# Optimization experiments

Measured on AMD Instinct MI355X. Metric: run time of the kernel, lower is better.

The kernel has to match this reference:

```python
import jax, jax.numpy as jnp
import numpy as np

N_P = 2048   # personality nodes
N_W = 89     # word nodes (fixed by user_word_adj[:, :89])
N_ALL = N_P + N_W
B = 16384    # users
E2 = 768     # sentence embedding size
UW = 313     # 89 word cols + 224 extra cols -> 32 + 224 = 256 for share1


def setup_inputs() -> dict:
    key = jax.random.key(0)
    ks = jax.random.split(key, 20)
    rn = lambda k, s, sc=0.1: (jax.random.normal(k, s, jnp.float32) * sc)
    pern_adj = jax.random.randint(ks[2], (N_P, N_P), 0, 2, jnp.int32)
    pern_adj = pern_adj.at[jnp.arange(N_P), jnp.arange(N_P)].set(1)
    word_pern_adj = jax.random.randint(ks[3], (N_ALL, N_ALL), 0, 2, jnp.int32)
    word_pern_adj = word_pern_adj.at[jnp.arange(N_ALL), jnp.arange(N_ALL)].set(1)
    return dict(
        pern_feature=rn(ks[0], (N_P, 256), 1.0),
        word_feature=rn(ks[1], (N_W, 256), 1.0),
        pern_adj=pern_adj,
        word_pern_adj=word_pern_adj,
        user_word_adj=jax.random.uniform(ks[4], (B, UW), jnp.float32),
        sentence_embed=rn(ks[5], (B, E2), 1.0),
        w1=rn(ks[6], (8, 256, 32)), a_src1=rn(ks[7], (8, 32)), a_dst1=rn(ks[8], (8, 32)), bias1=jnp.zeros((32,), jnp.float32),
        w2=rn(ks[9], (8, 256, 32)), a_src2=rn(ks[10], (8, 32)), a_dst2=rn(ks[11], (8, 32)), bias2=jnp.zeros((32,), jnp.float32),
        W_s1=rn(ks[12], (256, 128)), b_s1=jnp.zeros((128,), jnp.float32),
        W_s2=rn(ks[13], (E2, 128)), b_s2=jnp.zeros((128,), jnp.float32),
        W_f1=rn(ks[14], (128, 64)), b_f1=jnp.zeros((64,), jnp.float32),
        W_fa=rn(ks[15], (256, 128)), b_fa=jnp.zeros((128,), jnp.float32),
        W_fb=rn(ks[16], (128, 5)), b_fb=jnp.zeros((5,), jnp.float32),
    )


def gat(h, adj, w, a_src, a_dst, bias):
    # h: (n, f_in); w: (H, f_in, f_out); a_src/a_dst: (H, f_out); adj: (n, n) 0/1
    hp = jnp.einsum('nf,hfo->hno', h, w)                      # (H, n, f_out)
    e_src = jnp.einsum('hno,ho->hn', hp, a_src)               # (H, n)
    e_dst = jnp.einsum('hno,ho->hn', hp, a_dst)               # (H, n)
    e = jax.nn.leaky_relu(e_src[:, :, None] + e_dst[:, None, :], 0.2)  # (H, n, n)
    e = jnp.where(adj[None, :, :] > 0, e, jnp.float32(-1e9))
    attn = jax.nn.softmax(e, axis=-1)
    out = jnp.einsum('hnm,hmo->hno', attn, hp) + bias         # (H, n, f_out)
    return out, attn


def reference(pern_feature, word_feature, pern_adj, word_pern_adj,
              user_word_adj, sentence_embed,
              w1, a_src1, a_dst1, bias1, w2, a_src2, a_dst2, bias2,
              W_s1, b_s1, W_s2, b_s2, W_f1, b_f1, W_fa, b_fa, W_fb, b_fb):
    n_p = pern_feature.shape[0]
    # GAT 1 on personality graph
    h1, attn_pp = gat(pern_feature, pern_adj, w1, a_src1, a_dst1, bias1)
    h1 = jax.nn.elu(jnp.transpose(h1, (1, 0, 2)).reshape(n_p, -1))   # (n_p, 256)
    # dropout is identity at eval time
    h1_wp = jnp.concatenate([word_feature, h1], axis=0)               # (n_w+n_p, 256)
    # GAT 2 on word-personality graph, mean over heads
    h2, attn_wp = gat(h1_wp, word_pern_adj, w2, a_src2, a_dst2, bias2)
    h2 = h2.mean(axis=0)                                              # (n_w+n_p, 32)
    h2_word = h2[:word_feature.shape[0], :]                           # (89, 32)
    # user aggregation over word adjacency + row normalization
    x = user_word_adj[:, :N_W] @ h2_word                              # (B, 32)
    x_c = jnp.concatenate([x, user_word_adj[:, N_W:]], axis=1)        # (B, 256)
    x = x_c / x_c.sum(axis=1, keepdims=True)
    # dual heads
    output1 = x @ W_s1 + b_s1
    output2 = sentence_embed @ W_s2 + b_s2
    output1_new = output1 @ W_f1 + b_f1
    output2_new = output2 @ W_f1 + b_f1
    x_temp = jnp.concatenate([output1, output2], axis=1)
    x_temp = jax.nn.relu(x_temp @ W_fa + b_fa) @ W_fb + b_fb
    return (output1_new, output2_new, x_temp, attn_pp, attn_wp, x)
```

## Files before the change

### kernel.cpp

```cpp
#include <hip/hip_runtime.h>
#include <cstdint>
#include <cstddef>

#define N_P 2048
#define N_W 89
#define N_ALLC 2137
#define BQ 16384
#define E2C 768

typedef __attribute__((ext_vector_type(8))) short short8;
typedef __attribute__((ext_vector_type(4))) float float4v;

__device__ __forceinline__ float waveMax(float v){
#pragma unroll
  for (int o = 32; o > 0; o >>= 1) v = fmaxf(v, __shfl_down(v, o, 64));
  return v;
}
__device__ __forceinline__ float waveSum(float v){
#pragma unroll
  for (int o = 32; o > 0; o >>= 1) v += __shfl_down(v, o, 64);
  return v;
}
__device__ __forceinline__ unsigned short f2bf(float f){
  union { float f; unsigned int u; } v; v.f = f;
  unsigned int u = v.u;
  unsigned int r = (u + 0x7FFFu + ((u >> 16) & 1u)) >> 16;
  return (unsigned short)r;
}
__device__ __forceinline__ short8 cvt8(const float* p){
  float4 f0 = *(const float4*)p;
  float4 f1 = *(const float4*)(p + 4);
  short8 a;
  a[0] = (short)f2bf(f0.x); a[1] = (short)f2bf(f0.y);
  a[2] = (short)f2bf(f0.z); a[3] = (short)f2bf(f0.w);
  a[4] = (short)f2bf(f1.x); a[5] = (short)f2bf(f1.y);
  a[6] = (short)f2bf(f1.z); a[7] = (short)f2bf(f1.w);
  return a;
}

__device__ __forceinline__ void wpk_one(const float* __restrict__ W,
                                        unsigned short* __restrict__ out,
                                        int K, int N, int idx){
  if (idx >= K * N) return;
  int k = idx / N, n = idx - k * N;
  out[((size_t)((k >> 5) * 4 + ((k >> 3) & 3)) * N + n) * 8 + (k & 7)] = f2bf(W[idx]);
}

__global__ __launch_bounds__(256) void repack_all(
    const float* __restrict__ Ws1, unsigned short* __restrict__ ws1pk,
    const float* __restrict__ Ws2, unsigned short* __restrict__ ws2pk,
    const float* __restrict__ Wf1, unsigned short* __restrict__ wf1pk,
    const float* __restrict__ Wfa, unsigned short* __restrict__ wfapk,
    const float* __restrict__ wf, float* __restrict__ h1wp)
{
  int b = blockIdx.x, t = threadIdx.x;
  if (b < 128) {
    wpk_one(Ws1, ws1pk, 256, 128, b * 256 + t);
  } else if (b < 512) {
    wpk_one(Ws2, ws2pk, 768, 128, (b - 128) * 256 + t);
  } else if (b < 544) {
    wpk_one(Wf1, wf1pk, 128, 64, (b - 512) * 256 + t);
  } else if (b < 672) {
    wpk_one(Wfa, wfapk, 256, 128, (b - 544) * 256 + t);
  } else {
    int idx = (b - 672) * 256 + t;
    if (idx < N_W * 256) h1wp[idx] = wf[idx];
  }
}

__device__ __forceinline__ void gemm32_body(
    const float* __restrict__ A, int lda, int M,
    const float* __restrict__ w8,
    float* __restrict__ C, int ldc,
    int rt, int ct)
{
  __shared__ __align__(16) float As[16][36];
  __shared__ __align__(16) float Bs[16][68];
  int t = threadIdx.x;
  int m0 = rt * 32, n0 = ct * 64;
  int bk = t >> 4, bn = (t & 15) * 4;
  int tm = t >> 4, tn = t & 15;
  float acc[2][4] = {};
  for (int k0 = 0; k0 < 256; k0 += 16) {
    if (t < 128) {
      int ar = t >> 2, ak = (t & 3) * 4;
      float4 av = {0.f, 0.f, 0.f, 0.f};
      int arow = m0 + ar;
      if (arow < M) av = *(const float4*)(A + (size_t)arow * lda + k0 + ak);
      As[ak][ar] = av.x; As[ak + 1][ar] = av.y; As[ak + 2][ar] = av.z; As[ak + 3][ar] = av.w;
    }
    int n = n0 + bn;
    float4 bv = *(const float4*)(w8 + ((n >> 5) << 13) + ((k0 + bk) << 5) + (n & 31));
    *(float4*)&Bs[bk][bn] = bv;
    __syncthreads();
#pragma unroll
    for (int kk = 0; kk < 16; ++kk) {
      float a0 = As[kk][tm * 2], a1 = As[kk][tm * 2 + 1];
      float4 b4 = *(const float4*)&Bs[kk][tn * 4];
      acc[0][0] += a0 * b4.x; acc[0][1] += a0 * b4.y;
      acc[0][2] += a0 * b4.z; acc[0][3] += a0 * b4.w;
      acc[1][0] += a1 * b4.x; acc[1][1] += a1 * b4.y;
      acc[1][2] += a1 * b4.z; acc[1][3] += a1 * b4.w;
    }
    __syncthreads();
  }
#pragma unroll
  for (int i = 0; i < 2; ++i) {
    int row = m0 + tm * 2 + i;
    if (row < M) {
      float4 v;
      v.x = acc[i][0]; v.y = acc[i][1]; v.z = acc[i][2]; v.w = acc[i][3];
      *(float4*)(C + (size_t)row * ldc + n0 + tn * 4) = v;
    }
  }
}

__global__ __launch_bounds__(256) void hp1_o2(
    const float* __restrict__ pf, const float* __restrict__ w1,
    float* __restrict__ hp1,
    const float* __restrict__ sent, const unsigned short* __restrict__ ws2pk,
    const float* __restrict__ bs2, unsigned short* __restrict__ o12bf)
{
  int b = blockIdx.x, t = threadIdx.x;
  if (b < 256) {
    gemm32_body(pf, 256, N_P, w1, hp1, 256, b >> 2, b & 3);
    return;
  }
  int rb = b - 256;
  int w = t >> 6, lane = t & 63;
  int col = lane & 15, quad = lane >> 4;
  int rowA = rb * 64 + w * 16 + col;
  const float* A = sent + (size_t)rowA * E2C;
  float4v acc[8];
#pragma unroll
  for (int i = 0; i < 8; ++i) acc[i] = (float4v){0.f, 0.f, 0.f, 0.f};
#pragma unroll 4
  for (int k0 = 0; k0 < E2C; k0 += 32) {
    short8 a = cvt8(A + k0 + quad * 8);
    const unsigned short* wb = ws2pk + ((size_t)((k0 >> 5) * 4 + quad) * 128 + col) * 8;
#pragma unroll
    for (int nt = 0; nt < 8; ++nt)
      acc[nt] = __builtin_amdgcn_mfma_f32_16x16x32_bf16(a, *(const short8*)(wb + nt * 128), acc[nt], 0, 0, 0);
  }
  int rbase = rb * 64 + w * 16 + quad * 4;
#pragma unroll
  for (int nt = 0; nt < 8; ++nt) {
    int c = nt * 16 + col;
    float bv = bs2[c];
#pragma unroll
    for (int r = 0; r < 4; ++r)
      o12bf[(size_t)(rbase + r) * 256 + 128 + c] = f2bf(acc[nt][r] + bv);
  }
}

__global__ __launch_bounds__(256) void gemm_hp2(
    const float* __restrict__ h1wp, const float* __restrict__ w2,
    float* __restrict__ hp2)
{
  int b = blockIdx.x;
  gemm32_body(h1wp, 256, N_ALLC, w2, hp2, 256, b >> 2, b & 3);
}

__global__ __launch_bounds__(256) void esrc_edst(
    const float* __restrict__ hp,
    const float* __restrict__ a_src,
    const float* __restrict__ a_dst,
    float* __restrict__ es, float* __restrict__ ed,
    unsigned short* __restrict__ hppk,
    float* __restrict__ h2w, const float* __restrict__ b2,
    int N, int do_pack)
{
  __shared__ float sa[256], sd[256];
  int t = threadIdx.x;
  sa[t] = a_src[t]; sd[t] = a_dst[t];
  __syncthreads();
  int idx = blockIdx.x * 256 + t;
  if (h2w != nullptr && idx < N_W * 32) h2w[idx] = b2[idx & 31];
  if (idx >= N * 8) return;
  int n = idx >> 3, h = idx & 7;
  const float* hpp = hp + (size_t)n * 256 + h * 32;
  const float* ap = sa + h * 32;
  const float* dp = sd + h * 32;
  float s = 0.f, d = 0.f;
  float hv[32];
#pragma unroll
  for (int o = 0; o < 32; ++o) { hv[o] = hpp[o]; s += hv[o] * ap[o]; d += hv[o] * dp[o]; }
  es[h * N + n] = s; ed[h * N + n] = d;
  if (do_pack) {
    unsigned short* dst = hppk + (size_t)h * (N_P * 32)
                        + (size_t)((n >> 5) * 4 + ((n >> 3) & 3)) * 256 + (n & 7);
#pragma unroll
    for (int o = 0; o < 32; ++o) dst[o * 8] = f2bf(hv[o]);
  }
}

__global__ __launch_bounds__(256) void attn_softmax(
    const float* __restrict__ es, const float* __restrict__ ed,
    const int* __restrict__ adj,
    float* __restrict__ attn,
    int N)
{
  int h = blockIdx.x, n = blockIdx.y;
  int t = threadIdx.x, lane = t & 63, wid = t >> 6;
  __shared__ float red[4];
  float esv = es[h * N + n];
  const float* edh = ed + (size_t)h * N;
  const int* arow = adj + (size_t)n * N;
  float v[9];
  float lmax = -3e38f;
#pragma unroll
  for (int i = 0; i < 9; ++i) {
    int m = i * 256 + t;
    float x = -3e38f;
    if (m < N) {
      float e = esv + edh[m];
      e = (e >= 0.f) ? e : 0.2f * e;
      x = (arow[m] > 0) ? e : -1e9f;
    }
    v[i] = x; lmax = fmaxf(lmax, x);
  }
  lmax = waveMax(lmax);
  if (lane == 0) red[wid] = lmax;
  __syncthreads();
  float gmax = fmaxf(fmaxf(red[0], red[1]), fmaxf(red[2], red[3]));
  __syncthreads();
  float lsum = 0.f;
#pragma unroll
  for (int i = 0; i < 9; ++i) {
    int m = i * 256 + t;
    if (m < N) { float p = __expf(v[i] - gmax); v[i] = p; lsum += p; }
  }
  lsum = waveSum(lsum);
  if (lane == 0) red[wid] = lsum;
  __syncthreads();
  float inv = 1.f / (red[0] + red[1] + red[2] + red[3]);
  float* out = attn + ((size_t)h * N + n) * N;
#pragma unroll
  for (int i = 0; i < 9; ++i) {
    int m = i * 256 + t;
    if (m < N) out[m] = v[i] * inv;
  }
}

__global__ __launch_bounds__(256) void pv1_mfma(
    const float* __restrict__ attn,
    const unsigned short* __restrict__ hppk,
    const float* __restrict__ bias,
    float* __restrict__ h1wp)
{
  __shared__ float red[2][16][33];
  int t = threadIdx.x, w = t >> 6, lane = t & 63;
  int col = lane & 15, quad = lane >> 4;
  int kh = w >> 1, rh = (w & 1) * 16;
  int h = blockIdx.y;
  int row0 = blockIdx.x * 32;
  int rowA = row0 + rh + col;
  const float* arow = attn + ((size_t)h * N_P + rowA) * N_P + kh * 1024;
  const unsigned short* wb0 = hppk + (size_t)h * (N_P * 32) + (size_t)kh * 32768;
  float4v acc0 = {0.f, 0.f, 0.f, 0.f}, acc1 = {0.f, 0.f, 0.f, 0.f};
#pragma unroll 4
  for (int kk = 0; kk < 1024; kk += 32) {
    short8 a = cvt8(arow + kk + quad * 8);
    const unsigned short* wb = wb0 + ((size_t)((kk >> 5) * 4 + quad) * 32 + col) * 8;
    short8 b0 = *(const short8*)(wb);
    short8 b1 = *(const short8*)(wb + 128);
    acc0 = __builtin_amdgcn_mfma_f32_16x16x32_bf16(a, b0, acc0, 0, 0, 0);
    acc1 = __builtin_amdgcn_mfma_f32_16x16x32_bf16(a, b1, acc1, 0, 0, 0);
  }
  if (kh == 1) {
#pragma unroll
    for (int r = 0; r < 4; ++r) {
      red[w & 1][quad * 4 + r][col] = acc0[r];
      red[w & 1][quad * 4 + r][16 + col] = acc1[r];
    }
  }
  __syncthreads();
  if (kh == 0) {
    int rbase = row0 + rh + quad * 4;
#pragma unroll
    for (int r = 0; r < 4; ++r) {
      float v0 = acc0[r] + red[w & 1][quad * 4 + r][col] + bias[col];
      float v1 = acc1[r] + red[w & 1][quad * 4 + r][16 + col] + bias[16 + col];
      v0 = (v0 > 0.f) ? v0 : expm1f(v0);
      v1 = (v1 > 0.f) ? v1 : expm1f(v1);
      float* dst = h1wp + (size_t)(N_W + rbase + r) * 256 + h * 32;
      dst[col] = v0; dst[16 + col] = v1;
    }
  }
}

__global__ __launch_bounds__(256) void pv2(
    const float* __restrict__ attn,
    const float* __restrict__ hp,
    float* __restrict__ h2w)
{
  int n = blockIdx.x, h = blockIdx.y;
  int t = threadIdx.x, g = t >> 5, o = t & 31;
  const float* arow = attn + ((size_t)h * N_ALLC + n) * N_ALLC;
  float acc = 0.f;
  for (int m = g; m < N_ALLC; m += 8) acc += arow[m] * hp[(size_t)m * 256 + h * 32 + o];
  __shared__ float pv[8][33];
  pv[g][o] = acc;
  __syncthreads();
  if (t < 32) {
    float s = 0.f;
#pragma unroll
    for (int gg = 0; gg < 8; ++gg) s += pv[gg][t];
    atomicAdd(&h2w[n * 32 + t], s * 0.125f);
  }
}

__global__ __launch_bounds__(256) void xnorm_kernel(
    const float* __restrict__ uwa,
    const float* __restrict__ h2w,
    float* __restrict__ xout)
{
  __shared__ float urow[4][320];
  __shared__ float sh2w[N_W * 32];
  __shared__ float px[4][2][32];
  __shared__ float xh[4][33];
  __shared__ float inv[4];
  int t = threadIdx.x;
  int b0 = blockIdx.x * 4;
  for (int i = t; i < N_W * 32; i += 256) sh2w[i] = h2w[i];
  for (int idx = t; idx < 4 * 313; idx += 256) {
    int r = idx / 313, j = idx - r * 313;
    urow[r][j] = uwa[(size_t)(b0 + r) * 313 + j];
  }
  __syncthreads();
  {
    int r = t >> 6, q = (t >> 5) & 1, o = t & 31;
    float s = 0.f;
    int i0 = q * 45, i1 = q ? N_W : 45;
    for (int i = i0; i < i1; ++i) s += urow[r][i] * sh2w[i * 32 + o];
    px[r][q][o] = s;
  }
  __syncthreads();
  if (t < 128) {
    int r = t >> 5, o = t & 31;
    xh[r][o] = px[r][0][o] + px[r][1][o];
  }
  __syncthreads();
  int lane = t & 63, w = t >> 6;
  float ls = 0.f;
  for (int c = lane; c < 256; c += 64) {
    float v = (c < 32) ? xh[w][c] : urow[w][89 + c - 32];
    ls += v;
  }
  ls = waveSum(ls);
  if (lane == 0) inv[w] = 1.f / ls;
  __syncthreads();
  for (int idx = t; idx < 1024; idx += 256) {
    int r = idx >> 8, c = idx & 255;
    float v = (c < 32) ? xh[r][c] : urow[r][89 + c - 32];
    xout[(size_t)(b0 + r) * 256 + c] = v * inv[r];
  }
}

__global__ __launch_bounds__(256) void tail2(
    const float* __restrict__ x,
    const unsigned short* __restrict__ o12bf,
    const unsigned short* __restrict__ ws1pk,
    const unsigned short* __restrict__ wf1pk,
    const unsigned short* __restrict__ wfapk,
    const float* __restrict__ bs1,
    const float* __restrict__ bf1,
    const float* __restrict__ bfa,
    const float* __restrict__ Wfb,
    const float* __restrict__ bfb,
    float* __restrict__ o1n, float* __restrict__ o2n, float* __restrict__ xt)
{
  __shared__ unsigned short o12s[64][264];
  __shared__ float sWfb[640];
  int t = threadIdx.x, w = t >> 6, lane = t & 63;
  int col = lane & 15, quad = lane >> 4;
  int row0 = blockIdx.x * 64;
  for (int i = t; i < 640; i += 256) sWfb[i] = Wfb[i];
#pragma unroll
  for (int i = 0; i < 4; ++i) {
    int cid = t + i * 256;
    int r = cid >> 4, c8 = cid & 15;
    *(short8*)&o12s[r][128 + c8 * 8] =
        *(const short8*)(o12bf + (size_t)(row0 + r) * 256 + 128 + c8 * 8);
  }
  {
    int rowA = row0 + w * 16 + col;
    const float* A = x + (size_t)rowA * 256;
    float4v acc[8];
#pragma unroll
    for (int i = 0; i < 8; ++i) acc[i] = (float4v){0.f, 0.f, 0.f, 0.f};
#pragma unroll
    for (int k0 = 0; k0 < 256; k0 += 32) {
      short8 a = cvt8(A + k0 + quad * 8);
      const unsigned short* wb = ws1pk + ((size_t)((k0 >> 5) * 4 + quad) * 128 + col) * 8;
#pragma unroll
      for (int nt = 0; nt < 8; ++nt)
        acc[nt] = __builtin_amdgcn_mfma_f32_16x16x32_bf16(a, *(const short8*)(wb + nt * 128), acc[nt], 0, 0, 0);
    }
    int rb = w * 16 + quad * 4;
#pragma unroll
    for (int nt = 0; nt < 8; ++nt) {
      int c = nt * 16 + col;
      float bv = bs1[c];
#pragma unroll
      for (int r = 0; r < 4; ++r)
        o12s[rb + r][c] = f2bf(acc[nt][r] + bv);
    }
  }
  __syncthreads();
  int lr = w * 16 + col;
  float4v aT[8], a1[4], a2[4];
#pragma unroll
  for (int i = 0; i < 8; ++i) aT[i] = (float4v){0.f, 0.f, 0.f, 0.f};
#pragma unroll
  for (int i = 0; i < 4; ++i) { a1[i] = (float4v){0.f, 0.f, 0.f, 0.f}; a2[i] = (float4v){0.f, 0.f, 0.f, 0.f}; }
#pragma unroll
  for (int k0 = 0; k0 < 128; k0 += 32) {
    short8 a = *(const short8*)&o12s[lr][k0 + quad * 8];
    const unsigned short* wbT = wfapk + ((size_t)((k0 >> 5) * 4 + quad) * 128 + col) * 8;
    const unsigned short* wb1 = wf1pk + ((size_t)((k0 >> 5) * 4 + quad) * 64 + col) * 8;
#pragma unroll
    for (int nt = 0; nt < 8; ++nt)
      aT[nt] = __builtin_amdgcn_mfma_f32_16x16x32_bf16(a, *(const short8*)(wbT + nt * 128), aT[nt], 0, 0, 0);
#pragma unroll
    for (int nt = 0; nt < 4; ++nt)
      a1[nt] = __builtin_amdgcn_mfma_f32_16x16x32_bf16(a, *(const short8*)(wb1 + nt * 128), a1[nt], 0, 0, 0);
  }
#pragma unroll
  for (int k0 = 128; k0 < 256; k0 += 32) {
    short8 a = *(const short8*)&o12s[lr][k0 + quad * 8];
    const unsigned short* wbT = wfapk + ((size_t)((k0 >> 5) * 4 + quad) * 128 + col) * 8;
    const unsigned short* wb1 = wf1pk + ((size_t)(((k0 - 128) >> 5) * 4 + quad) * 64 + col) * 8;
#pragma unroll
    for (int nt = 0; nt < 8; ++nt)
      aT[nt] = __builtin_amdgcn_mfma_f32_16x16x32_bf16(a, *(const short8*)(wbT + nt * 128), aT[nt], 0, 0, 0);
#pragma unroll
    for (int nt = 0; nt < 4; ++nt)
      a2[nt] = __builtin_amdgcn_mfma_f32_16x16x32_bf16(a, *(const short8*)(wb1 + nt * 128), a2[nt], 0, 0, 0);
  }
  int rbase = row0 + w * 16 + quad * 4;
#pragma unroll
  for (int nt = 0; nt < 4; ++nt) {
    int c = nt * 16 + col;
    float b1v = bf1[c];
#pragma unroll
    for (int r = 0; r < 4; ++r) {
      o1n[(size_t)(rbase + r) * 64 + c] = a1[nt][r] + b1v;
      o2n[(size_t)(rbase + r) * 64 + c] = a2[nt][r] + b1v;
    }
  }
  float xp[4][5] = {};
#pragma unroll
  for (int nt = 0; nt < 8; ++nt) {
    int c = nt * 16 + col;
    float bav = bfa[c];
#pragma unroll
    for (int r = 0; r < 4; ++r) {
      float tv = fmaxf(aT[nt][r] + bav, 0.f);
#pragma unroll
      for (int q = 0; q < 5; ++q) xp[r][q] += tv * sWfb[c * 5 + q];
    }
  }
#pragma unroll
  for (int m = 1; m <= 8; m <<= 1) {
#pragma unroll
    for (int r = 0; r < 4; ++r)
#pragma unroll
      for (int q = 0; q < 5; ++q) xp[r][q] += __shfl_xor(xp[r][q], m, 64);
  }
  if (col == 0) {
#pragma unroll
    for (int r = 0; r < 4; ++r)
#pragma unroll
      for (int q = 0; q < 5; ++q) xt[(size_t)(rbase + r) * 5 + q] = xp[r][q] + bfb[q];
  }
}

extern "C" void kernel_launch(void* const* d_in, const int* in_sizes, int n_in,
                              void* d_out, int out_size, void* d_ws, size_t ws_size,
                              hipStream_t stream)
{
  const float* pf   = (const float*)d_in[0];
  const float* wf   = (const float*)d_in[1];
  const int*   adj1 = (const int*)d_in[2];
  const int*   adj2 = (const int*)d_in[3];
  const float* uwa  = (const float*)d_in[4];
  const float* sent = (const float*)d_in[5];
  const float* w1   = (const float*)d_in[6];
  const float* as1  = (const float*)d_in[7];
  const float* ad1  = (const float*)d_in[8];
  const float* b1   = (const float*)d_in[9];
  const float* w2   = (const float*)d_in[10];
  const float* as2  = (const float*)d_in[11];
  const float* ad2  = (const float*)d_in[12];
  const float* b2   = (const float*)d_in[13];
  const float* Ws1  = (const float*)d_in[14];
  const float* bs1  = (const float*)d_in[15];
  const float* Ws2  = (const float*)d_in[16];
  const float* bs2  = (const float*)d_in[17];
  const float* Wf1  = (const float*)d_in[18];
  const float* bf1  = (const float*)d_in[19];
  const float* Wfa  = (const float*)d_in[20];
  const float* bfa  = (const float*)d_in[21];
  const float* Wfb  = (const float*)d_in[22];
  const float* bfb  = (const float*)d_in[23];

  float* ws = (float*)d_ws;
  float* hp1  = ws;
  float* hp2  = hp1 + (size_t)N_P * 256;
  float* es1v = hp2 + (size_t)N_ALLC * 256;
  float* ed1v = es1v + 8 * N_P;
  float* es2v = ed1v + 8 * N_P;
  float* ed2v = es2v + 17152;
  float* h1wp = ed2v + 17152;
  float* h2w  = h1wp + (size_t)N_ALLC * 256;
  unsigned short* o12bf = (unsigned short*)(h2w + 2880);
  unsigned short* hp1pk = o12bf + (size_t)BQ * 256;
  unsigned short* ws1pk = hp1pk + 8 * N_P * 32;
  unsigned short* ws2pk = ws1pk + 256 * 128;
  unsigned short* wf1pk = ws2pk + 768 * 128;
  unsigned short* wfapk = wf1pk + 128 * 64;

  float* out = (float*)d_out;
  float* out_o1n = out;
  float* out_o2n = out + (size_t)BQ * 64;
  float* out_xt  = out + (size_t)BQ * 128;
  float* out_app = out_xt + (size_t)BQ * 5;
  float* out_awp = out_app + (size_t)8 * N_P * N_P;
  float* out_x   = out_awp + (size_t)8 * N_ALLC * N_ALLC;

  repack_all<<<761, 256, 0, stream>>>(Ws1, ws1pk, Ws2, ws2pk, Wf1, wf1pk, Wfa, wfapk, wf, h1wp);
  hp1_o2<<<512, 256, 0, stream>>>(pf, w1, hp1, sent, ws2pk, bs2, o12bf);
  esrc_edst<<<(N_P * 8 + 255) / 256, 256, 0, stream>>>(hp1, as1, ad1, es1v, ed1v,
                                                       hp1pk, nullptr, nullptr, N_P, 1);
  attn_softmax<<<dim3(8, N_P), 256, 0, stream>>>(es1v, ed1v, adj1, out_app, N_P);
  pv1_mfma<<<dim3(64, 8), 256, 0, stream>>>(out_app, hp1pk, b1, h1wp);
  gemm_hp2<<<268, 256, 0, stream>>>(h1wp, w2, hp2);
  esrc_edst<<<(N_ALLC * 8 + 255) / 256, 256, 0, stream>>>(hp2, as2, ad2, es2v, ed2v,
                                                          nullptr, h2w, b2, N_ALLC, 0);
  attn_softmax<<<dim3(8, N_ALLC), 256, 0, stream>>>(es2v, ed2v, adj2, out_awp, N_ALLC);
  pv2<<<dim3(N_W, 8), 256, 0, stream>>>(out_awp, hp2, h2w);
  xnorm_kernel<<<BQ / 4, 256, 0, stream>>>(uwa, h2w, out_x);
  tail2<<<BQ / 64, 256, 0, stream>>>(out_x, o12bf, ws1pk, wf1pk, wfapk,
                                     bs1, bf1, bfa, Wfb, bfb,
                                     out_o1n, out_o2n, out_xt);
}
```

Baseline: 786.2 us.

## Pack adjacency into bitmasks, widen GEMM tiles, split tail into two kernels

New measurement: 722.4 us. 1.09x faster.

```diff
diff --git a/kernel.cpp b/kernel.cpp
--- a/kernel.cpp
+++ b/kernel.cpp
@@ -51,7 +51,9 @@
     const float* __restrict__ Ws2, unsigned short* __restrict__ ws2pk,
     const float* __restrict__ Wf1, unsigned short* __restrict__ wf1pk,
     const float* __restrict__ Wfa, unsigned short* __restrict__ wfapk,
-    const float* __restrict__ wf, float* __restrict__ h1wp)
+    const float* __restrict__ wf, float* __restrict__ h1wp,
+    const int* __restrict__ adj1, unsigned long long* __restrict__ bm1,
+    const int* __restrict__ adj2, unsigned long long* __restrict__ bm2)
 {
   int b = blockIdx.x, t = threadIdx.x;
   if (b < 128) {
@@ -62,51 +64,74 @@
     wpk_one(Wf1, wf1pk, 128, 64, (b - 512) * 256 + t);
   } else if (b < 672) {
     wpk_one(Wfa, wfapk, 256, 128, (b - 544) * 256 + t);
-  } else {
+  } else if (b < 761) {
     int idx = (b - 672) * 256 + t;
     if (idx < N_W * 256) h1wp[idx] = wf[idx];
-  }
-}
-
-__device__ __forceinline__ void gemm32_body(
+  } else if (b < 1017) {
+    int r0 = (b - 761) * 8;
+    int wv = t >> 6, ln = t & 63;
+    for (int rr = 0; rr < 8; ++rr) {
+      int r = r0 + rr;
+      const int* arow = adj1 + (size_t)r * N_P;
+      for (int m0 = wv * 64; m0 < N_P; m0 += 256) {
+        unsigned long long mask = __ballot(arow[m0 + ln] > 0);
+        if (ln == 0) bm1[(size_t)r * 32 + (m0 >> 6)] = mask;
+      }
+    }
+  } else {
+    int r0 = (b - 1017) * 8;
+    int wv = t >> 6, ln = t & 63;
+    for (int rr = 0; rr < 8; ++rr) {
+      int r = r0 + rr;
+      if (r >= N_ALLC) break;
+      const int* arow = adj2 + (size_t)r * N_ALLC;
+      for (int m0 = wv * 64; m0 < 2176; m0 += 256) {
+        int m = m0 + ln;
+        unsigned long long mask = __ballot((m < N_ALLC) && (arow[m] > 0));
+        if (ln == 0) bm2[(size_t)r * 34 + (m0 >> 6)] = mask;
+      }
+    }
+  }
+}
+
+__device__ __forceinline__ void gemm_w_body(
     const float* __restrict__ A, int lda, int M,
     const float* __restrict__ w8,
     float* __restrict__ C, int ldc,
     int rt, int ct)
 {
-  __shared__ __align__(16) float As[16][36];
+  __shared__ __align__(16) float As[16][68];
   __shared__ __align__(16) float Bs[16][68];
   int t = threadIdx.x;
-  int m0 = rt * 32, n0 = ct * 64;
+  int m0 = rt * 64, n0 = ct * 64;
+  int tm = t >> 4, tn = t & 15;
+  int ar = t >> 2, ak = (t & 3) * 4;
   int bk = t >> 4, bn = (t & 15) * 4;
-  int tm = t >> 4, tn = t & 15;
-  float acc[2][4] = {};
+  float acc[4][4] = {};
   for (int k0 = 0; k0 < 256; k0 += 16) {
-    if (t < 128) {
-      int ar = t >> 2, ak = (t & 3) * 4;
-      float4 av = {0.f, 0.f, 0.f, 0.f};
-      int arow = m0 + ar;
-      if (arow < M) av = *(const float4*)(A + (size_t)arow * lda + k0 + ak);
-      As[ak][ar] = av.x; As[ak + 1][ar] = av.y; As[ak + 2][ar] = av.z; As[ak + 3][ar] = av.w;
-    }
+    float4 av = {0.f, 0.f, 0.f, 0.f};
+    int arow = m0 + ar;
+    if (arow < M) av = *(const float4*)(A + (size_t)arow * lda + k0 + ak);
+    As[ak][ar] = av.x; As[ak + 1][ar] = av.y; As[ak + 2][ar] = av.z; As[ak + 3][ar] = av.w;
     int n = n0 + bn;
-    float4 bv = *(const float4*)(w8 + ((n >> 5) << 13) + ((k0 + bk) << 5) + (n & 31));
-    *(float4*)&Bs[bk][bn] = bv;
+    *(float4*)&Bs[bk][bn] = *(const float4*)(w8 + ((n >> 5) << 13) + ((k0 + bk) << 5) + (n & 31));
     __syncthreads();
 #pragma unroll
     for (int kk = 0; kk < 16; ++kk) {
-      float a0 = As[kk][tm * 2], a1 = As[kk][tm * 2 + 1];
+      float4 a4 = *(const float4*)&As[kk][tm * 4];
       float4 b4 = *(const float4*)&Bs[kk][tn * 4];
-      acc[0][0] += a0 * b4.x; acc[0][1] += a0 * b4.y;
-      acc[0][2] += a0 * b4.z; acc[0][3] += a0 * b4.w;
-      acc[1][0] += a1 * b4.x; acc[1][1] += a1 * b4.y;
-      acc[1][2] += a1 * b4.z; acc[1][3] += a1 * b4.w;
+      float a[4] = {a4.x, a4.y, a4.z, a4.w};
+      float b[4] = {b4.x, b4.y, b4.z, b4.w};
+#pragma unroll
+      for (int i = 0; i < 4; ++i)
+#pragma unroll
+        for (int j = 0; j < 4; ++j) acc[i][j] += a[i] * b[j];
     }
     __syncthreads();
   }
 #pragma unroll
-  for (int i = 0; i < 2; ++i) {
-    int row = m0 + tm * 2 + i;
+  for (int i = 0; i < 4; ++i) {
+    int row = m0 + tm * 4 + i;
     if (row < M) {
       float4 v;
       v.x = acc[i][0]; v.y = acc[i][1]; v.z = acc[i][2]; v.w = acc[i][3];
@@ -122,11 +147,11 @@
     const float* __restrict__ bs2, unsigned short* __restrict__ o12bf)
 {
   int b = blockIdx.x, t = threadIdx.x;
-  if (b < 256) {
-    gemm32_body(pf, 256, N_P, w1, hp1, 256, b >> 2, b & 3);
+  if (b < 128) {
+    gemm_w_body(pf, 256, N_P, w1, hp1, 256, b >> 2, b & 3);
     return;
   }
-  int rb = b - 256;
+  int rb = b - 128;
   int w = t >> 6, lane = t & 63;
   int col = lane & 15, quad = lane >> 4;
   int rowA = rb * 64 + w * 16 + col;
@@ -157,8 +182,7 @@
     const float* __restrict__ h1wp, const float* __restrict__ w2,
     float* __restrict__ hp2)
 {
-  int b = blockIdx.x;
-  gemm32_body(h1wp, 256, N_ALLC, w2, hp2, 256, b >> 2, b & 3);
+  gemm_w_body(h1wp, 256, N_ALLC, w2, hp2, 256, blockIdx.x, blockIdx.y);
 }
 
 __global__ __launch_bounds__(256) void esrc_edst(
@@ -196,7 +220,7 @@
 
 __global__ __launch_bounds__(256) void attn_softmax(
     const float* __restrict__ es, const float* __restrict__ ed,
-    const int* __restrict__ adj,
+    const unsigned long long* __restrict__ bm, int bstride,
     float* __restrict__ attn,
     int N)
 {
@@ -205,7 +229,7 @@
   __shared__ float red[4];
   float esv = es[h * N + n];
   const float* edh = ed + (size_t)h * N;
-  const int* arow = adj + (size_t)n * N;
+  const unsigned long long* brow = bm + (size_t)n * bstride;
   float v[9];
   float lmax = -3e38f;
 #pragma unroll
@@ -215,7 +239,7 @@
     if (m < N) {
       float e = esv + edh[m];
       e = (e >= 0.f) ? e : 0.2f * e;
-      x = (arow[m] > 0) ? e : -1e9f;
+      x = ((brow[m >> 6] >> (m & 63)) & 1ULL) ? e : -1e9f;
     }
     v[i] = x; lmax = fmaxf(lmax, x);
   }
@@ -357,58 +381,56 @@
   }
 }
 
-__global__ __launch_bounds__(256) void tail2(
+__global__ __launch_bounds__(256) void o1_gemm(
     const float* __restrict__ x,
+    const unsigned short* __restrict__ ws1pk,
+    const float* __restrict__ bs1,
+    unsigned short* __restrict__ o12bf)
+{
+  int t = threadIdx.x, w = t >> 6, lane = t & 63;
+  int col = lane & 15, quad = lane >> 4;
+  int rowA = blockIdx.x * 64 + w * 16 + col;
+  const float* A = x + (size_t)rowA * 256;
+  float4v acc[8];
+#pragma unroll
+  for (int i = 0; i < 8; ++i) acc[i] = (float4v){0.f, 0.f, 0.f, 0.f};
+#pragma unroll
+  for (int k0 = 0; k0 < 256; k0 += 32) {
+    short8 a = cvt8(A + k0 + quad * 8);
+    const unsigned short* wb = ws1pk + ((size_t)((k0 >> 5) * 4 + quad) * 128 + col) * 8;
+#pragma unroll
+    for (int nt = 0; nt < 8; ++nt)
+      acc[nt] = __builtin_amdgcn_mfma_f32_16x16x32_bf16(a, *(const short8*)(wb + nt * 128), acc[nt], 0, 0, 0);
+  }
+  int rbase = blockIdx.x * 64 + w * 16 + quad * 4;
+#pragma unroll
+  for (int nt = 0; nt < 8; ++nt) {
+    int c = nt * 16 + col;
+    float bv = bs1[c];
+#pragma unroll
+    for (int r = 0; r < 4; ++r)
+      o12bf[(size_t)(rbase + r) * 256 + c] = f2bf(acc[nt][r] + bv);
+  }
+}
+
+__global__ __launch_bounds__(256) void tail_fused(
     const unsigned short* __restrict__ o12bf,
-    const unsigned short* __restrict__ ws1pk,
     const unsigned short* __restrict__ wf1pk,
     const unsigned short* __restrict__ wfapk,
-    const float* __restrict__ bs1,
     const float* __restrict__ bf1,
     const float* __restrict__ bfa,
     const float* __restrict__ Wfb,
     const float* __restrict__ bfb,
     float* __restrict__ o1n, float* __restrict__ o2n, float* __restrict__ xt)
 {
-  __shared__ unsigned short o12s[64][264];
   __shared__ float sWfb[640];
-  int t = threadIdx.x, w = t >> 6, lane = t & 63;
+  int t = threadIdx.x;
+  for (int i = t; i < 640; i += 256) sWfb[i] = Wfb[i];
+  __syncthreads();
+  int w = t >> 6, lane = t & 63;
   int col = lane & 15, quad = lane >> 4;
-  int row0 = blockIdx.x * 64;
-  for (int i = t; i < 640; i += 256) sWfb[i] = Wfb[i];
-#pragma unroll
-  for (int i = 0; i < 4; ++i) {
-    int cid = t + i * 256;
-    int r = cid >> 4, c8 = cid & 15;
-    *(short8*)&o12s[r][128 + c8 * 8] =
-        *(const short8*)(o12bf + (size_t)(row0 + r) * 256 + 128 + c8 * 8);
-  }
-  {
-    int rowA = row0 + w * 16 + col;
-    const float* A = x + (size_t)rowA * 256;
-    float4v acc[8];
-#pragma unroll
-    for (int i = 0; i < 8; ++i) acc[i] = (float4v){0.f, 0.f, 0.f, 0.f};
-#pragma unroll
-    for (int k0 = 0; k0 < 256; k0 += 32) {
-      short8 a = cvt8(A + k0 + quad * 8);
-      const unsigned short* wb = ws1pk + ((size_t)((k0 >> 5) * 4 + quad) * 128 + col) * 8;
-#pragma unroll
-      for (int nt = 0; nt < 8; ++nt)
-        acc[nt] = __builtin_amdgcn_mfma_f32_16x16x32_bf16(a, *(const short8*)(wb + nt * 128), acc[nt], 0, 0, 0);
-    }
-    int rb = w * 16 + quad * 4;
-#pragma unroll
-    for (int nt = 0; nt < 8; ++nt) {
-      int c = nt * 16 + col;
-      float bv = bs1[c];
-#pragma unroll
-      for (int r = 0; r < 4; ++r)
-        o12s[rb + r][c] = f2bf(acc[nt][r] + bv);
-    }
-  }
-  __syncthreads();
-  int lr = w * 16 + col;
+  int rowA = blockIdx.x * 64 + w * 16 + col;
+  const unsigned short* ar = o12bf + (size_t)rowA * 256;
   float4v aT[8], a1[4], a2[4];
 #pragma unroll
   for (int i = 0; i < 8; ++i) aT[i] = (float4v){0.f, 0.f, 0.f, 0.f};
@@ -416,7 +438,7 @@
   for (int i = 0; i < 4; ++i) { a1[i] = (float4v){0.f, 0.f, 0.f, 0.f}; a2[i] = (float4v){0.f, 0.f, 0.f, 0.f}; }
 #pragma unroll
   for (int k0 = 0; k0 < 128; k0 += 32) {
-    short8 a = *(const short8*)&o12s[lr][k0 + quad * 8];
+    short8 a = *(const short8*)(ar + k0 + quad * 8);
     const unsigned short* wbT = wfapk + ((size_t)((k0 >> 5) * 4 + quad) * 128 + col) * 8;
     const unsigned short* wb1 = wf1pk + ((size_t)((k0 >> 5) * 4 + quad) * 64 + col) * 8;
 #pragma unroll
@@ -428,7 +450,7 @@
   }
 #pragma unroll
   for (int k0 = 128; k0 < 256; k0 += 32) {
-    short8 a = *(const short8*)&o12s[lr][k0 + quad * 8];
+    short8 a = *(const short8*)(ar + k0 + quad * 8);
     const unsigned short* wbT = wfapk + ((size_t)((k0 >> 5) * 4 + quad) * 128 + col) * 8;
     const unsigned short* wb1 = wf1pk + ((size_t)(((k0 - 128) >> 5) * 4 + quad) * 64 + col) * 8;
 #pragma unroll
@@ -438,7 +460,7 @@
     for (int nt = 0; nt < 4; ++nt)
       a2[nt] = __builtin_amdgcn_mfma_f32_16x16x32_bf16(a, *(const short8*)(wb1 + nt * 128), a2[nt], 0, 0, 0);
   }
-  int rbase = row0 + w * 16 + quad * 4;
+  int rbase = blockIdx.x * 64 + w * 16 + quad * 4;
 #pragma unroll
   for (int nt = 0; nt < 4; ++nt) {
     int c = nt * 16 + col;
@@ -514,7 +536,9 @@
   float* ed2v = es2v + 17152;
   float* h1wp = ed2v + 17152;
   float* h2w  = h1wp + (size_t)N_ALLC * 256;
-  unsigned short* o12bf = (unsigned short*)(h2w + 2880);
+  unsigned long long* bm1 = (unsigned long long*)(h2w + 2880);
+  unsigned long long* bm2 = bm1 + (size_t)2048 * 32;
+  unsigned short* o12bf = (unsigned short*)(bm2 + 72704);
   unsigned short* hp1pk = o12bf + (size_t)BQ * 256;
   unsigned short* ws1pk = hp1pk + 8 * N_P * 32;
   unsigned short* ws2pk = ws1pk + 256 * 128;
@@ -529,19 +553,20 @@
   float* out_awp = out_app + (size_t)8 * N_P * N_P;
   float* out_x   = out_awp + (size_t)8 * N_ALLC * N_ALLC;
 
-  repack_all<<<761, 256, 0, stream>>>(Ws1, ws1pk, Ws2, ws2pk, Wf1, wf1pk, Wfa, wfapk, wf, h1wp);
-  hp1_o2<<<512, 256, 0, stream>>>(pf, w1, hp1, sent, ws2pk, bs2, o12bf);
+  repack_all<<<1285, 256, 0, stream>>>(Ws1, ws1pk, Ws2, ws2pk, Wf1, wf1pk, Wfa, wfapk,
+                                       wf, h1wp, adj1, bm1, adj2, bm2);
+  hp1_o2<<<384, 256, 0, stream>>>(pf, w1, hp1, sent, ws2pk, bs2, o12bf);
   esrc_edst<<<(N_P * 8 + 255) / 256, 256, 0, stream>>>(hp1, as1, ad1, es1v, ed1v,
                                                        hp1pk, nullptr, nullptr, N_P, 1);
-  attn_softmax<<<dim3(8, N_P), 256, 0, stream>>>(es1v, ed1v, adj1, out_app, N_P);
+  attn_softmax<<<dim3(8, N_P), 256, 0, stream>>>(es1v, ed1v, bm1, 32, out_app, N_P);
   pv1_mfma<<<dim3(64, 8), 256, 0, stream>>>(out_app, hp1pk, b1, h1wp);
-  gemm_hp2<<<268, 256, 0, stream>>>(h1wp, w2, hp2);
+  gemm_hp2<<<dim3(34, 4), 256, 0, stream>>>(h1wp, w2, hp2);
   esrc_edst<<<(N_ALLC * 8 + 255) / 256, 256, 0, stream>>>(hp2, as2, ad2, es2v, ed2v,
                                                           nullptr, h2w, b2, N_ALLC, 0);
-  attn_softmax<<<dim3(8, N_ALLC), 256, 0, stream>>>(es2v, ed2v, adj2, out_awp, N_ALLC);
+  attn_softmax<<<dim3(8, N_ALLC), 256, 0, stream>>>(es2v, ed2v, bm2, 34, out_awp, N_ALLC);
   pv2<<<dim3(N_W, 8), 256, 0, stream>>>(out_awp, hp2, h2w);
   xnorm_kernel<<<BQ / 4, 256, 0, stream>>>(uwa, h2w, out_x);
-  tail2<<<BQ / 64, 256, 0, stream>>>(out_x, o12bf, ws1pk, wf1pk, wfapk,
-                                     bs1, bf1, bfa, Wfb, bfb,
-                                     out_o1n, out_o2n, out_xt);
-}
+  o1_gemm<<<BQ / 64, 256, 0, stream>>>(out_x, ws1pk, bs1, o12bf);
+  tail_fused<<<BQ / 64, 256, 0, stream>>>(o12bf, wf1pk, wfapk, bf1, bfa, Wfb, bfb,
+                                          out_o1n, out_o2n, out_xt);
+}
```
